# Performance work log

Hardware: AMD Instinct MI355X
Metric: run time of the kernel (lower is better)

Reference implementation:

```python
import jax, jax.numpy as jnp
import numpy as np

N, P, B, F, M, L, H = 10000, 25000, 8, 16, 32, 2, 2  # nodes, edge-pairs, batch, feats, MLP_feats, n_layers, MLP_layers


def setup_inputs() -> dict:
    key = jax.random.key(0)
    rng = np.random.default_rng(0)
    u = rng.integers(0, N, size=P)
    v = rng.integers(0, N, size=P)
    # E = 2P+1: forward pairs, reversed pairs, one fixed edge (matches cat([eff,-eff,fixed]))
    src = jnp.asarray(np.concatenate([u, v, [0]]), dtype=jnp.int32)
    dst = jnp.asarray(np.concatenate([v, u, [0]]), dtype=jnp.int32)
    ks = jax.random.split(key, 14)
    w = lambda k, shape, fan: jax.random.normal(k, shape, jnp.float32) * (fan ** -0.5)
    b = lambda k, shape: jax.random.normal(k, shape, jnp.float32) * 0.01
    return {
        'h': jax.random.normal(ks[0], (B, N, F), jnp.float32),
        # per-edge-pair (interactive) MLP params, stacked over n_layers L
        'Wi0': w(ks[1], (L, P, 2 * F, M), 2 * F),
        'Wih': w(ks[2], (L, H, P, M, M), M),
        'Wiout': w(ks[3], (L, P, M, F), M),
        'bi0': b(ks[4], (L, P, 1, M)),
        'bih': b(ks[5], (L, H, P, 1, M)),
        'biout': b(ks[6], (L, P, 1, F)),
        # shared (fixed-edge) MLP params
        'Wf0': w(ks[7], (L, 1, 2 * F, M), 2 * F),
        'Wfh': w(ks[8], (L, H, 1, M, M), M),
        'Wfout': w(ks[9], (L, 1, M, F), M),
        'bf0': b(ks[10], (L, 1, 1, M)),
        'bfh': b(ks[11], (L, H, 1, 1, M)),
        'bfout': b(ks[12], (L, 1, 1, F)),
        'src': src,
        'dst': dst,
    }


def _edge_mlp(x, W0, Wh, Wout, b0, bh, bout):
    # x: [P,B,2F]; batched per-edge MLP with SiLU hidden activations
    y = jax.nn.silu(jnp.einsum('pbf,pfm->pbm', x, W0) + b0)
    for i in range(Wh.shape[0]):
        y = jax.nn.silu(jnp.einsum('pbf,pfm->pbm', y, Wh[i]) + bh[i])
    return jnp.einsum('pbf,pfm->pbm', y, Wout) + bout


def reference(h, Wi0, Wih, Wiout, bi0, bih, biout, Wf0, Wfh, Wfout, bf0, bfh, bfout, src, dst):
    n_nodes = h.shape[1]
    E = src.shape[0]
    p = (E - 1) // 2
    x = jnp.transpose(h, (1, 0, 2))  # [N,B,F] (torch permute(1,0,2))
    for l in range(Wi0.shape[0]):
        # gather only the edges actually used: first P pairs + the final fixed edge
        e_eff = jnp.concatenate([x[dst[:p]], x[src[:p]]], axis=-1)   # [P,B,2F]
        e_fix = jnp.concatenate([x[dst[-1:]], x[src[-1:]]], axis=-1)  # [1,B,2F]
        eff = _edge_mlp(e_eff, Wi0[l], Wih[l], Wiout[l], bi0[l], bih[l], biout[l])
        fx = _edge_mlp(e_fix, Wf0[l], Wfh[l], Wfout[l], bf0[l], bfh[l], bfout[l])
        msgs = jnp.concatenate([eff, -eff, fx], axis=0)  # [E,B,F]
        x = jax.ops.segment_sum(msgs, dst, num_segments=n_nodes)  # sum-reduce onto dst nodes
    return jnp.transpose(x, (1, 0, 2))  # back to [B,N,F]
```

## Files before the change

### kernel.cpp

```cpp
#include <hip/hip_runtime.h>

#define BB 8
#define FF 16
#define MM 32
#define TF 32
#define ROW 40

__device__ __forceinline__ float silu_f(float x) {
    return x / (1.0f + __expf(-x));
}

__device__ __forceinline__ float4 dense32(const float* __restrict__ Wp, int rstride,
                                          const float a[TF], float4 acc) {
#pragma unroll
    for (int k = 0; k < TF; ++k) {
        const float4 wv = *(const float4*)(Wp + k * rstride);
        acc.x += a[k] * wv.x;
        acc.y += a[k] * wv.y;
        acc.z += a[k] * wv.z;
        acc.w += a[k] * wv.w;
    }
    return acc;
}

__device__ __forceinline__ void load_row(const float* arow, float a[TF]) {
#pragma unroll
    for (int c = 0; c < 8; ++c) {
        const float4 t = *(const float4*)(arow + 4 * c);
        a[4 * c + 0] = t.x;
        a[4 * c + 1] = t.y;
        a[4 * c + 2] = t.z;
        a[4 * c + 3] = t.w;
    }
}

extern "C" __global__ void __launch_bounds__(256) gnn_edge_kernel(
    const float* __restrict__ x_in, float* __restrict__ x_out,
    const float* __restrict__ Wi0, const float* __restrict__ Wih,
    const float* __restrict__ Wiout, const float* __restrict__ bi0,
    const float* __restrict__ bih, const float* __restrict__ biout,
    const float* __restrict__ Wf0, const float* __restrict__ Wfh,
    const float* __restrict__ Wfout, const float* __restrict__ bf0,
    const float* __restrict__ bfh, const float* __restrict__ bfout,
    const int* __restrict__ src, const int* __restrict__ dst,
    int P, int E, int H,
    long in_ns, long in_bs,
    long out_ns, long out_bs)
{
    __shared__ float act[4][BB * ROW];

    const int w    = threadIdx.x >> 6;
    const int lane = threadIdx.x & 63;
    const int b    = lane >> 3;
    const int lg   = lane & 7;
    const int cg   = lg & 3;

    const bool isFixed = (blockIdx.x == (int)gridDim.x - 1);
    if (isFixed && w != 0) return;

    int p, nd, ns;
    const float *W0p, *Whp, *Woutp, *b0p, *bhp, *boutp;
    long whstride, bhstride;
    if (isFixed) {
        W0p = Wf0; Whp = Wfh; Woutp = Wfout;
        b0p = bf0; bhp = bfh; boutp = bfout;
        whstride = (long)(MM * MM);
        bhstride = (long)MM;
        nd = dst[E - 1];
        ns = src[E - 1];
    } else {
        p = blockIdx.x * 4 + w;
        if (p >= P) return;
        W0p   = Wi0   + (long)p * (TF * MM);
        Whp   = Wih   + (long)p * (MM * MM);
        Woutp = Wiout + (long)p * (MM * FF);
        b0p   = bi0   + (long)p * MM;
        bhp   = bih   + (long)p * MM;
        boutp = biout + (long)p * FF;
        whstride = (long)P * (MM * MM);
        bhstride = (long)P * MM;
        nd = dst[p];
        ns = src[p];
    }

    float* arow = &act[w][b * ROW];

    {
        const int   gnode = (lg < 4) ? nd : ns;
        const float* gp = x_in + (long)gnode * in_ns + (long)b * in_bs + cg * 4;
        const float4 g = *(const float4*)gp;
        *(float4*)(arow + ((lg < 4) ? 0 : FF) + cg * 4) = g;
    }

    float a[TF];
    float4 r;

    load_row(arow, a);
    r = dense32(W0p + lg * 4, MM, a, *(const float4*)(b0p + lg * 4));
    r.x = silu_f(r.x); r.y = silu_f(r.y); r.z = silu_f(r.z); r.w = silu_f(r.w);
    *(float4*)(arow + lg * 4) = r;

    for (int i = 0; i < H; ++i) {
        load_row(arow, a);
        r = dense32(Whp + (long)i * whstride + lg * 4, MM, a,
                    *(const float4*)(bhp + (long)i * bhstride + lg * 4));
        r.x = silu_f(r.x); r.y = silu_f(r.y); r.z = silu_f(r.z); r.w = silu_f(r.w);
        *(float4*)(arow + lg * 4) = r;
    }

    load_row(arow, a);
    r = dense32(Woutp + cg * 4, FF, a, *(const float4*)(boutp + cg * 4));

    const bool pos = (lg < 4);
    if (isFixed && !pos) return;
    const int   node = pos ? nd : ns;
    const float s    = pos ? 1.0f : -1.0f;
    float* op = x_out + (long)node * out_ns + (long)b * out_bs + cg * 4;
    atomicAdd(op + 0, s * r.x);
    atomicAdd(op + 1, s * r.y);
    atomicAdd(op + 2, s * r.z);
    atomicAdd(op + 3, s * r.w);
}

extern "C" void kernel_launch(void* const* d_in, const int* in_sizes, int n_in,
                              void* d_out, int out_size, void* d_ws, size_t ws_size,
                              hipStream_t stream)
{
    const float* h     = (const float*)d_in[0];
    const float* Wi0   = (const float*)d_in[1];
    const float* Wih   = (const float*)d_in[2];
    const float* Wiout = (const float*)d_in[3];
    const float* bi0   = (const float*)d_in[4];
    const float* bih   = (const float*)d_in[5];
    const float* biout = (const float*)d_in[6];
    const float* Wf0   = (const float*)d_in[7];
    const float* Wfh   = (const float*)d_in[8];
    const float* Wfout = (const float*)d_in[9];
    const float* bf0   = (const float*)d_in[10];
    const float* bfh   = (const float*)d_in[11];
    const float* bfout = (const float*)d_in[12];
    const int*   src   = (const int*)d_in[13];
    const int*   dst   = (const int*)d_in[14];

    const int E = in_sizes[13];
    const int P = (E - 1) / 2;
    const int N = in_sizes[0] / (BB * FF);
    const int L = (int)((long)in_sizes[1] / ((long)P * TF * MM));
    const int H = (int)((long)in_sizes[2] / ((long)L * P * MM * MM));

    float* ws0 = (float*)d_ws;
    float* ws1 = ws0 + (long)N * BB * FF;

    const int blocksE = (P + 3) / 4;
    dim3 grid(blocksE + 1), block(256);

    for (int l = 0; l < L; ++l) {
        const float* xin;
        long ins_n, ins_b;
        if (l == 0) { xin = h; ins_n = FF; ins_b = (long)N * FF; }
        else        { xin = (l % 2 == 1) ? ws0 : ws1; ins_n = BB * FF; ins_b = FF; }

        float* xout;
        long outs_n, outs_b;
        if (l == L - 1) { xout = (float*)d_out; outs_n = FF; outs_b = (long)N * FF; }
        else            { xout = (l % 2 == 0) ? ws0 : ws1; outs_n = BB * FF; outs_b = FF; }

        hipMemsetAsync(xout, 0, (size_t)N * BB * FF * sizeof(float), stream);

        gnn_edge_kernel<<<grid, block, 0, stream>>>(
            xin, xout,
            Wi0   + (long)l * P * TF * MM,
            Wih   + (long)l * H * P * MM * MM,
            Wiout + (long)l * P * MM * FF,
            bi0   + (long)l * P * MM,
            bih   + (long)l * H * P * MM,
            biout + (long)l * P * FF,
            Wf0   + (long)l * TF * MM,
            Wfh   + (long)l * H * MM * MM,
            Wfout + (long)l * MM * FF,
            bf0   + (long)l * MM,
            bfh   + (long)l * H * MM,
            bfout + (long)l * FF,
            src, dst, P, E, H,
            ins_n, ins_b, outs_n, outs_b);
    }
}
```

Before: 891.6 us.

## Replace atomic scatter with CSR-based gather aggregation of edge messages

Edge kernel now writes per-pair messages to a buffer instead of issuing float atomics. A CSR adjacency keyed by destination is built each call with count, single-block scan and fill kernels. A separate aggregation kernel then gathers and sums the messages per node, which removes the per-layer memset. The costs are extra launches, a serial single-block scan over the nodes, an extra message buffer round trip, and a summation order that depends on the nondeterministic fill order.

New measurement: 936.4 us. 5.0% more time.

```diff
diff --git a/kernel.cpp b/kernel.cpp
--- a/kernel.cpp
+++ b/kernel.cpp
@@ -34,8 +34,55 @@
     }
 }
 
-extern "C" __global__ void __launch_bounds__(256) gnn_edge_kernel(
-    const float* __restrict__ x_in, float* __restrict__ x_out,
+
+extern "C" __global__ void count_kernel(const int* __restrict__ dst,
+                                        int* __restrict__ deg, int E) {
+    const int e = blockIdx.x * 256 + threadIdx.x;
+    if (e < E) atomicAdd(&deg[dst[e]], 1);
+}
+
+extern "C" __global__ void scan_kernel(const int* __restrict__ deg,
+                                       int* __restrict__ rowptr, int N) {
+    __shared__ int buf[256];
+    __shared__ int carry_s;
+    const int t = threadIdx.x;
+    if (t == 0) carry_s = 0;
+    __syncthreads();
+    for (int base = 0; base < N; base += 256) {
+        const int v = (base + t < N) ? deg[base + t] : 0;
+        buf[t] = v;
+        __syncthreads();
+#pragma unroll
+        for (int off = 1; off < 256; off <<= 1) {
+            const int tv = (t >= off) ? buf[t - off] : 0;
+            __syncthreads();
+            buf[t] += tv;
+            __syncthreads();
+        }
+        const int incl = buf[t];
+        const int carry = carry_s;
+        if (base + t < N) rowptr[base + t] = carry + incl - v;
+        __syncthreads();
+        if (t == 255) carry_s = carry + buf[255];
+        __syncthreads();
+    }
+    if (t == 0) rowptr[N] = carry_s;
+}
+
+extern "C" __global__ void fill_kernel(const int* __restrict__ dst,
+                                       const int* __restrict__ rowptr,
+                                       int* __restrict__ cursor,
+                                       int* __restrict__ adj, int E) {
+    const int e = blockIdx.x * 256 + threadIdx.x;
+    if (e < E) {
+        const int d = dst[e];
+        const int slot = atomicAdd(&cursor[d], 1);
+        adj[rowptr[d] + slot] = e;
+    }
+}
+
+extern "C" __global__ void __launch_bounds__(256, 3) gnn_edge_kernel(
+    const float* __restrict__ x_in, float* __restrict__ msg,
     const float* __restrict__ Wi0, const float* __restrict__ Wih,
     const float* __restrict__ Wiout, const float* __restrict__ bi0,
     const float* __restrict__ bih, const float* __restrict__ biout,
@@ -44,8 +91,7 @@
     const float* __restrict__ bfh, const float* __restrict__ bfout,
     const int* __restrict__ src, const int* __restrict__ dst,
     int P, int E, int H,
-    long in_ns, long in_bs,
-    long out_ns, long out_bs)
+    long in_ns, long in_bs)
 {
     __shared__ float act[4][BB * ROW];
 
@@ -58,7 +104,7 @@
     const bool isFixed = (blockIdx.x == (int)gridDim.x - 1);
     if (isFixed && w != 0) return;
 
-    int p, nd, ns;
+    int p, nd, ns, pmsg;
     const float *W0p, *Whp, *Woutp, *b0p, *bhp, *boutp;
     long whstride, bhstride;
     if (isFixed) {
@@ -68,6 +114,7 @@
         bhstride = (long)MM;
         nd = dst[E - 1];
         ns = src[E - 1];
+        pmsg = P;
     } else {
         p = blockIdx.x * 4 + w;
         if (p >= P) return;
@@ -81,12 +128,13 @@
         bhstride = (long)P * MM;
         nd = dst[p];
         ns = src[p];
+        pmsg = p;
     }
 
     float* arow = &act[w][b * ROW];
 
     {
-        const int   gnode = (lg < 4) ? nd : ns;
+        const int    gnode = (lg < 4) ? nd : ns;
         const float* gp = x_in + (long)gnode * in_ns + (long)b * in_bs + cg * 4;
         const float4 g = *(const float4*)gp;
         *(float4*)(arow + ((lg < 4) ? 0 : FF) + cg * 4) = g;
@@ -111,15 +159,34 @@
     load_row(arow, a);
     r = dense32(Woutp + cg * 4, FF, a, *(const float4*)(boutp + cg * 4));
 
-    const bool pos = (lg < 4);
-    if (isFixed && !pos) return;
-    const int   node = pos ? nd : ns;
-    const float s    = pos ? 1.0f : -1.0f;
-    float* op = x_out + (long)node * out_ns + (long)b * out_bs + cg * 4;
-    atomicAdd(op + 0, s * r.x);
-    atomicAdd(op + 1, s * r.y);
-    atomicAdd(op + 2, s * r.z);
-    atomicAdd(op + 3, s * r.w);
+    if (lg < 4) {
+        *(float4*)(msg + (long)pmsg * (BB * FF) + b * FF + cg * 4) = r;
+    }
+}
+
+extern "C" __global__ void __launch_bounds__(256) agg_kernel(
+    const float* __restrict__ msg, const int* __restrict__ rowptr,
+    const int* __restrict__ adj, float* __restrict__ x_out,
+    int N, int P, long out_ns, long out_bs)
+{
+    const int t = threadIdx.x;
+    const int n = blockIdx.x * 8 + (t >> 5);
+    if (n >= N) return;
+    const int b  = (t >> 2) & 7;
+    const int jj = t & 3;
+
+    float4 acc = {0.f, 0.f, 0.f, 0.f};
+    const int beg = rowptr[n], end = rowptr[n + 1];
+    for (int i = beg; i < end; ++i) {
+        const int e = adj[i];
+        int   idx = e;
+        float s   = 1.0f;
+        if (e >= P && e < 2 * P) { idx = e - P; s = -1.0f; }
+        else if (e == 2 * P)     { idx = P; }
+        const float4 v = *(const float4*)(msg + (long)idx * (BB * FF) + b * FF + jj * 4);
+        acc.x += s * v.x; acc.y += s * v.y; acc.z += s * v.z; acc.w += s * v.w;
+    }
+    *(float4*)(x_out + (long)n * out_ns + (long)b * out_bs + jj * 4) = acc;
 }
 
 extern "C" void kernel_launch(void* const* d_in, const int* in_sizes, int n_in,
@@ -148,27 +215,37 @@
     const int L = (int)((long)in_sizes[1] / ((long)P * TF * MM));
     const int H = (int)((long)in_sizes[2] / ((long)L * P * MM * MM));
 
-    float* ws0 = (float*)d_ws;
-    float* ws1 = ws0 + (long)N * BB * FF;
+    float* msg   = (float*)d_ws;
+    float* xmid0 = msg + (long)(P + 1) * BB * FF;
+    float* xmid1 = xmid0 + (long)N * BB * FF;
+    int*   deg    = (int*)(xmid1 + (long)N * BB * FF);
+    int*   cursor = deg + N;
+    int*   rowptr = cursor + N;
+    int*   adj    = rowptr + N + 1;
+
+    hipMemsetAsync(deg, 0, (size_t)(2 * N) * sizeof(int), stream);
+    const int eb = (E + 255) / 256;
+    count_kernel<<<eb, 256, 0, stream>>>(dst, deg, E);
+    scan_kernel<<<1, 256, 0, stream>>>(deg, rowptr, N);
+    fill_kernel<<<eb, 256, 0, stream>>>(dst, rowptr, cursor, adj, E);
 
     const int blocksE = (P + 3) / 4;
-    dim3 grid(blocksE + 1), block(256);
+    dim3 egrid(blocksE + 1), eblock(256);
+    dim3 agrid((N + 7) / 8), ablock(256);
 
     for (int l = 0; l < L; ++l) {
         const float* xin;
         long ins_n, ins_b;
         if (l == 0) { xin = h; ins_n = FF; ins_b = (long)N * FF; }
-        else        { xin = (l % 2 == 1) ? ws0 : ws1; ins_n = BB * FF; ins_b = FF; }
+        else        { xin = (l & 1) ? xmid0 : xmid1; ins_n = BB * FF; ins_b = FF; }
 
         float* xout;
         long outs_n, outs_b;
         if (l == L - 1) { xout = (float*)d_out; outs_n = FF; outs_b = (long)N * FF; }
-        else            { xout = (l % 2 == 0) ? ws0 : ws1; outs_n = BB * FF; outs_b = FF; }
-
-        hipMemsetAsync(xout, 0, (size_t)N * BB * FF * sizeof(float), stream);
-
-        gnn_edge_kernel<<<grid, block, 0, stream>>>(
-            xin, xout,
+        else            { xout = (l & 1) ? xmid1 : xmid0; outs_n = BB * FF; outs_b = FF; }
+
+        gnn_edge_kernel<<<egrid, eblock, 0, stream>>>(
+            xin, msg,
             Wi0   + (long)l * P * TF * MM,
             Wih   + (long)l * H * P * MM * MM,
             Wiout + (long)l * P * MM * FF,
@@ -182,6 +259,9 @@
             bfh   + (long)l * H * MM,
             bfout + (long)l * FF,
             src, dst, P, E, H,
-            ins_n, ins_b, outs_n, outs_b);
-    }
-}
+            ins_n, ins_b);
+
+        agg_kernel<<<agrid, ablock, 0, stream>>>(
+            msg, rowptr, adj, xout, N, P, outs_n, outs_b);
+    }
+}
```
